# Kernel tuning notes

Hardware: AMD Instinct MI355X
Metric: run time of the kernel (lower is better)

Reference implementation:

```python
import jax, jax.numpy as jnp
import numpy as np

B, HID, REC, NC, T = 512, 196, 488, 35, 120
BN_EPS = 1e-3


def _bn(x, g, b):
    # eval-mode CustomBatchNorm1d: running_mean=0, running_var=1
    return g * (x / jnp.sqrt(1.0 + BN_EPS)) + b


def _gru(x, Wih, Whh, bih, bhh):
    """Standard torch nn.GRU (batch_first), h0 = 0. x: [B,T,D] -> [B,T,H]."""
    H = Whh.shape[1]
    def step(h, xt):
        xg = xt @ Wih.T + bih          # [B,3H]
        hg = h @ Whh.T + bhh           # [B,3H]
        xr, xz, xn = jnp.split(xg, 3, axis=1)
        hr, hz, hn = jnp.split(hg, 3, axis=1)
        r = jax.nn.sigmoid(xr + hr)
        z = jax.nn.sigmoid(xz + hz)
        n = jnp.tanh(xn + r * hn)
        h2 = (1.0 - z) * n + z * h
        return h2, h2
    h0 = jnp.zeros((x.shape[0], H), x.dtype)
    _, ys = jax.lax.scan(step, h0, jnp.swapaxes(x, 0, 1))
    return jnp.swapaxes(ys, 0, 1)


def _custom_gru(x, Wih, Whh, bih):
    """CustomGRUCell (eval mode: prev_target=0 so weight_tf term vanishes)."""
    H = Whh.shape[1]
    Whh_rz = Whh[:2 * H]
    Whh_n = Whh[2 * H:]
    b_r, b_z, b_n = bih[:H], bih[H:2 * H], bih[2 * H:]
    def step(h, xt):
        xg = xt @ Wih.T                 # [B,3H], no bias in F.linear
        xr, xz, xn = jnp.split(xg, 3, axis=1)
        hg = h @ Whh_rz.T               # only r,z rows needed (h_h chunk unused)
        hr, hz = jnp.split(hg, 2, axis=1)
        r = jax.nn.sigmoid(xr + hr + b_r)
        u = jax.nn.sigmoid(xz + hz + b_z)
        n = jax.nn.softmax(xn + (r * h) @ Whh_n.T + b_n, axis=1)
        h2 = (1.0 - u) * n + u * h
        return h2, h2
    h0 = jnp.zeros((x.shape[0], H), x.dtype)
    _, ys = jax.lax.scan(step, h0, jnp.swapaxes(x, 0, 1))
    return jnp.swapaxes(ys, 0, 1)


def setup_inputs() -> dict:
    key = jax.random.key(0)
    ks = jax.random.split(key, 16)
    s = 0.05
    inp = {
        "z_in": jax.random.normal(ks[0], (B, HID), jnp.float32),
        "W0": jax.random.normal(ks[1], (HID, HID), jnp.float32) * s,
        "b0": jnp.zeros((HID,), jnp.float32),
        "g0": jnp.full((1, HID), 0.1, jnp.float32),
        "beta0": jnp.zeros((1, HID), jnp.float32),
        "W1": jax.random.normal(ks[2], (HID, HID), jnp.float32) * s,
        "b1": jnp.zeros((HID,), jnp.float32),
        "g1": jnp.full((1, HID), 0.1, jnp.float32),
        "beta1": jnp.zeros((1, HID), jnp.float32),
        "gru0_Wih": jax.random.normal(ks[3], (3 * REC, HID), jnp.float32) * s,
        "gru0_Whh": jax.random.normal(ks[4], (3 * REC, REC), jnp.float32) * s,
        "gru0_bih": jax.random.normal(ks[5], (3 * REC,), jnp.float32) * s,
        "gru0_bhh": jax.random.normal(ks[6], (3 * REC,), jnp.float32) * s,
        "gru1_Wih": jax.random.normal(ks[7], (3 * REC, REC), jnp.float32) * s,
        "gru1_Whh": jax.random.normal(ks[8], (3 * REC, REC), jnp.float32) * s,
        "gru1_bih": jax.random.normal(ks[9], (3 * REC,), jnp.float32) * s,
        "gru1_bhh": jax.random.normal(ks[10], (3 * REC,), jnp.float32) * s,
        "cell_Wih": jax.random.normal(ks[11], (3 * NC, REC), jnp.float32) * s,
        "cell_Whh": jax.random.normal(ks[12], (3 * NC, NC), jnp.float32) * s,
        "cell_bih": jax.random.normal(ks[13], (3 * NC,), jnp.float32) * s,
    }
    return inp


def reference(z_in, W0, b0, g0, beta0, W1, b1, g1, beta1,
              gru0_Wih, gru0_Whh, gru0_bih, gru0_bhh,
              gru1_Wih, gru1_Whh, gru1_bih, gru1_bhh,
              cell_Wih, cell_Whh, cell_bih):
    z = _bn(z_in @ W0.T + b0, g0, beta0)
    z = _bn(z @ W1.T + b1, g1, beta1)
    z_reps = jnp.broadcast_to(z[:, None, :], (z.shape[0], T, z.shape[1]))
    x = _gru(z_reps, gru0_Wih, gru0_Whh, gru0_bih, gru0_bhh)
    x = _gru(x, gru1_Wih, gru1_Whh, gru1_bih, gru1_bhh)
    x_out = _custom_gru(x, cell_Wih, cell_Whh, cell_bih)  # [B,T,NCHARS]
    return x_out
```

## Files before the change

### kernel.cpp

```cpp
#include <hip/hip_runtime.h>
#include <math.h>

#define Bsz 512
#define HID 196
#define REC 488
#define NC  35
#define TT  120
#define G3  1464
#define NSLOT 123

#define KT   8
#define NCH  61
#define NB   61
#define CELLB 32
#define NGRID (3*NB + CELLB)
#define WSL  (NCH*KT*24)

#define HWREG_XCC_ID (20 | (0 << 6) | (31 << 11))

struct CellSmem { float xs[16][492]; float hs[16][36]; float rh[16][36]; };

__device__ __forceinline__ float sigmoidf_(float x) { return 1.0f / (1.0f + __expf(-x)); }

__device__ __forceinline__ void gbar(int* bar, int target) {
  __syncthreads();
  if (threadIdx.x == 0) {
    __builtin_amdgcn_fence(__ATOMIC_RELEASE, "agent");
    __hip_atomic_fetch_add(bar, 1, __ATOMIC_RELAXED, __HIP_MEMORY_SCOPE_AGENT);
    while (__hip_atomic_load(bar, __ATOMIC_RELAXED, __HIP_MEMORY_SCOPE_AGENT) < target)
      __builtin_amdgcn_s_sleep(2);
    __builtin_amdgcn_fence(__ATOMIC_ACQUIRE, "agent");
  }
  __syncthreads();
}

__device__ __forceinline__ void gbar2(int* bar, int xcd, int cntx, int nx, int s) {
  __syncthreads();
  if (threadIdx.x == 0) {
    int* bar1 = bar + 32*(1 + xcd);
    int old = __hip_atomic_fetch_add(bar1, 1, __ATOMIC_RELAXED, __HIP_MEMORY_SCOPE_AGENT);
    if (old == cntx*(s+1) - 1) {
      __builtin_amdgcn_fence(__ATOMIC_RELEASE, "agent");
      __hip_atomic_fetch_add(bar, 1, __ATOMIC_RELAXED, __HIP_MEMORY_SCOPE_AGENT);
    }
    while (__hip_atomic_load(bar, __ATOMIC_RELAXED, __HIP_MEMORY_SCOPE_AGENT) < nx*(s+1))
      __builtin_amdgcn_s_sleep(2);
    __builtin_amdgcn_fence(__ATOMIC_ACQUIRE, "agent");
  }
  __syncthreads();
}

__global__ void dense_bn_kernel(const float* __restrict__ X, const float* __restrict__ W,
                                const float* __restrict__ bias, const float* __restrict__ g,
                                const float* __restrict__ beta, float* __restrict__ Y) {
  __shared__ float xs[HID];
  int b = blockIdx.x;
  for (int k = threadIdx.x; k < HID; k += blockDim.x) xs[k] = X[(size_t)b*HID + k];
  __syncthreads();
  int j = threadIdx.x;
  if (j < HID) {
    const float4* wr = (const float4*)(W + (size_t)j*HID);
    float acc = 0.f;
    #pragma unroll 7
    for (int k4 = 0; k4 < HID/4; ++k4) {
      float4 w4 = wr[k4];
      acc += xs[4*k4+0]*w4.x + xs[4*k4+1]*w4.y + xs[4*k4+2]*w4.z + xs[4*k4+3]*w4.w;
    }
    float v = (acc + bias[j]) * 0.9995003746f;
    Y[(size_t)b*HID + j] = g[j]*v + beta[j];
  }
}

__global__ __launch_bounds__(256)
void xg0v2_kernel(const float* __restrict__ Z, const float* __restrict__ Wih,
                  const float* __restrict__ bih, float* __restrict__ XGT) {
  __shared__ float zs[HID*4];
  int b0 = blockIdx.x << 2;
  for (int idx = threadIdx.x; idx < HID*4; idx += 256) {
    int k = idx >> 2, i = idx & 3;
    zs[idx] = Z[(size_t)(b0+i)*HID + k];
  }
  __syncthreads();
  for (int c = threadIdx.x; c < G3; c += 256) {
    const float4* wr = (const float4*)(Wih + (size_t)c*HID);
    float a0=0.f,a1=0.f,a2=0.f,a3=0.f;
    for (int k4 = 0; k4 < HID/4; ++k4) {
      float4 w = wr[k4];
      const float* zp = zs + (k4<<4);
      a0=fmaf(w.x,zp[0],a0);  a1=fmaf(w.x,zp[1],a1);  a2=fmaf(w.x,zp[2],a2);  a3=fmaf(w.x,zp[3],a3);
      a0=fmaf(w.y,zp[4],a0);  a1=fmaf(w.y,zp[5],a1);  a2=fmaf(w.y,zp[6],a2);  a3=fmaf(w.y,zp[7],a3);
      a0=fmaf(w.z,zp[8],a0);  a1=fmaf(w.z,zp[9],a1);  a2=fmaf(w.z,zp[10],a2); a3=fmaf(w.z,zp[11],a3);
      a0=fmaf(w.w,zp[12],a0); a1=fmaf(w.w,zp[13],a1); a2=fmaf(w.w,zp[14],a2); a3=fmaf(w.w,zp[15],a3);
    }
    float bb = bih[c];
    XGT[(size_t)c*Bsz + b0+0] = a0 + bb;
    XGT[(size_t)c*Bsz + b0+1] = a1 + bb;
    XGT[(size_t)c*Bsz + b0+2] = a2 + bb;
    XGT[(size_t)c*Bsz + b0+3] = a3 + bb;
  }
}

__global__ __launch_bounds__(256)
void wtrans_kernel(const float* __restrict__ Whh0, const float* __restrict__ Wih1,
                   const float* __restrict__ Whh1, float* __restrict__ Wt2) {
  int blk = blockIdx.x;
  int stage = blk / NB, j = blk - stage*NB;
  const float* Wsrc = (stage==0) ? Whh0 : (stage==1) ? Wih1 : Whh1;
  float* dst = Wt2 + (size_t)blk*WSL;
  for (int idx = threadIdx.x; idx < WSL; idx += 256) {
    int ck = idx / 192, rem = idx - ck*192;
    int k = rem / 24, r = rem - k*24;
    int g = r >> 3, cl = r & 7;
    dst[idx] = Wsrc[(size_t)(g*REC + j*8 + cl)*REC + ck*8 + k];
  }
}

__device__ __forceinline__ void gemm24s(const float* __restrict__ AT, int b,
                                        const float* __restrict__ wp,
                                        float (&acc)[24])
{
  float av[KT], nv[KT];
  #pragma unroll
  for (int k = 0; k < KT; ++k) av[k] = AT[(size_t)k*Bsz + b];
  for (int ck = 0; ck < NCH; ++ck) {
    if (ck + 1 < NCH) {
      const float* src = AT + (size_t)(ck+1)*KT*Bsz + b;
      #pragma unroll
      for (int k = 0; k < KT; ++k) nv[k] = src[(size_t)k*Bsz];
    }
    const float* w = wp + ck*192;
    #pragma unroll
    for (int k = 0; k < KT; ++k) {
      float a = av[k];
      #pragma unroll
      for (int r = 0; r < 24; ++r)
        acc[r] = fmaf(a, w[k*24 + r], acc[r]);
    }
    #pragma unroll
    for (int k = 0; k < KT; ++k) av[k] = nv[k];
  }
}

__global__ __launch_bounds__(512)
void pers_kernel(const float* __restrict__ xg0T,
                 float* __restrict__ h0T, float* __restrict__ h1T,
                 float* __restrict__ xg1T, float* __restrict__ hc,
                 float* __restrict__ out,
                 const float* __restrict__ Wt2,
                 const float* __restrict__ bhh0,
                 const float* __restrict__ bih1, const float* __restrict__ bhh1,
                 const float* __restrict__ cWih, const float* __restrict__ cWhh,
                 const float* __restrict__ cb, int* __restrict__ bar)
{
  __shared__ CellSmem S;
  const int blk = blockIdx.x;
  const int tid = threadIdx.x;
  const int stage = (blk < NB) ? 0 : (blk < 2*NB) ? 1 : (blk < 3*NB) ? 2 : 3;
  const int l = tid & 63, w = tid >> 6;
  const float* wslice = Wt2 + (size_t)blk*WSL;

  const int xcd = __builtin_amdgcn_s_getreg(HWREG_XCC_ID) & 7;
  if (tid == 0)
    __hip_atomic_fetch_add(bar + 32*(9 + xcd), 1, __ATOMIC_RELAXED, __HIP_MEMORY_SCOPE_AGENT);
  gbar(bar + 544, NGRID);
  int cntx = 0, nx = 0;
  if (tid == 0) {
    cntx = __hip_atomic_load(bar + 32*(9 + xcd), __ATOMIC_RELAXED, __HIP_MEMORY_SCOPE_AGENT);
    #pragma unroll
    for (int x = 0; x < 8; ++x)
      nx += (__hip_atomic_load(bar + 32*(9 + x), __ATOMIC_RELAXED, __HIP_MEMORY_SCOPE_AGENT) > 0);
  }

  for (int s = 0; s < NSLOT; ++s) {
    if (stage == 0) {
      if (s < TT) {
        int j = blk;
        const float* hprevT = h0T + (size_t)((s+1)&1)*REC*Bsz;
        float*       hnewT  = h0T + (size_t)(s&1)*REC*Bsz;
        float acc[24] = {0};
        gemm24s(hprevT, tid, wslice, acc);
        int b = tid, c0 = j*8;
        #pragma unroll
        for (int cl = 0; cl < 8; ++cl) {
          int c = c0 + cl;
          float xrv = xg0T[(size_t)c*Bsz + b];
          float xzv = xg0T[(size_t)(REC+c)*Bsz + b];
          float xnv = xg0T[(size_t)(2*REC+c)*Bsz + b];
          float r = sigmoidf_(xrv + acc[cl]      + bhh0[c]);
          float z = sigmoidf_(xzv + acc[8+cl]    + bhh0[REC+c]);
          float n = tanhf   (xnv + r*(acc[16+cl] + bhh0[2*REC+c]));
          hnewT[(size_t)c*Bsz + b] = (1.f-z)*n + z*hprevT[(size_t)c*Bsz + b];
        }
      }
    } else if (stage == 1) {
      if (s >= 1 && s <= TT) {
        int t1 = s - 1;
        const float* xT   = h0T  + (size_t)(t1&1)*REC*Bsz;
        float*       xgwT = xg1T + (size_t)(t1&1)*G3*Bsz;
        float acc[24] = {0};
        gemm24s(xT, tid, wslice, acc);
        int b = tid, c0 = (blk - NB)*8;
        #pragma unroll
        for (int cl = 0; cl < 8; ++cl) {
          int c = c0 + cl;
          xgwT[(size_t)c*Bsz + b]         = acc[cl];
          xgwT[(size_t)(REC+c)*Bsz + b]   = acc[8+cl];
          xgwT[(size_t)(2*REC+c)*Bsz + b] = acc[16+cl];
        }
      }
    } else if (stage == 2) {
      if (s >= 2 && s <= TT+1) {
        int t2 = s - 2;
        const float* hprevT = h1T  + (size_t)((t2+1)&1)*REC*Bsz;
        float*       hnewT  = h1T  + (size_t)(t2&1)*REC*Bsz;
        const float* xgrT   = xg1T + (size_t)(t2&1)*G3*Bsz;
        float acc[24] = {0};
        gemm24s(hprevT, tid, wslice, acc);
        int b = tid, c0 = (blk - 2*NB)*8;
        #pragma unroll
        for (int cl = 0; cl < 8; ++cl) {
          int c = c0 + cl;
          float xrv = xgrT[(size_t)c*Bsz + b];
          float xzv = xgrT[(size_t)(REC+c)*Bsz + b];
          float xnv = xgrT[(size_t)(2*REC+c)*Bsz + b];
          float r = sigmoidf_(xrv + acc[cl]   + bih1[c]     + bhh1[c]);
          float z = sigmoidf_(xzv + acc[8+cl] + bih1[REC+c] + bhh1[REC+c]);
          float n = tanhf   (xnv + bih1[2*REC+c] + r*(acc[16+cl] + bhh1[2*REC+c]));
          hnewT[(size_t)c*Bsz + b] = (1.f-z)*n + z*hprevT[(size_t)c*Bsz + b];
        }
      }
    } else {
      if (s >= 3) {
        int t3 = s - 3;
        int b0 = (blk - 3*NB) << 4;
        const float* xT = h1T + (size_t)(t3&1)*REC*Bsz;
        const float* hp = hc  + (size_t)((t3+1)&1)*Bsz*NC;
        float*       hn = hc  + (size_t)(t3&1)*Bsz*NC;
        for (int idx = tid; idx < 16*REC; idx += 512) {
          int k = idx >> 4, it = idx & 15;
          S.xs[it][k] = xT[(size_t)k*Bsz + b0 + it];
        }
        if (l < NC) {
          #pragma unroll
          for (int q = 0; q < 2; ++q) {
            int it = (w<<1) + q;
            S.hs[it][l] = hp[(size_t)(b0+it)*NC + l];
          }
        }
        __syncthreads();
        for (int q = 0; q < 2; ++q) {
          int it = (w<<1) + q;
          int b = b0 + it;
          float v = -1e30f, u = 0.f, hpc = 0.f;
          if (l < NC) {
            const float4* wr4 = (const float4*)(cWih + (size_t)l*REC);
            const float4* wz4 = (const float4*)(cWih + (size_t)(NC+l)*REC);
            const float4* wn4 = (const float4*)(cWih + (size_t)(2*NC+l)*REC);
            const float4* xs4 = (const float4*)(S.xs[it]);
            float xr=0.f, xz=0.f, xn=0.f;
            #pragma unroll 2
            for (int k4 = 0; k4 < REC/4; ++k4) {
              float4 xv = xs4[k4];
              float4 wa = wr4[k4], wb = wz4[k4], wc = wn4[k4];
              xr += wa.x*xv.x + wa.y*xv.y + wa.z*xv.z + wa.w*xv.w;
              xz += wb.x*xv.x + wb.y*xv.y + wb.z*xv.z + wb.w*xv.w;
              xn += wc.x*xv.x + wc.y*xv.y + wc.z*xv.z + wc.w*xv.w;
            }
            float hr=0.f, hz=0.f;
            for (int k = 0; k < NC; ++k) {
              float hv = S.hs[it][k];
              hr = fmaf(hv, cWhh[(size_t)l*NC + k], hr);
              hz = fmaf(hv, cWhh[(size_t)(NC+l)*NC + k], hz);
            }
            float r = sigmoidf_(xr + hr + cb[l]);
            u       = sigmoidf_(xz + hz + cb[NC+l]);
            hpc = S.hs[it][l];
            S.rh[it][l] = r * hpc;
            v = xn;
          }
          __syncthreads();
          if (l < NC) {
            float hnn = 0.f;
            for (int k = 0; k < NC; ++k)
              hnn = fmaf(S.rh[it][k], cWhh[(size_t)(2*NC+l)*NC + k], hnn);
            v = v + hnn + cb[2*NC+l];
          }
          float m = v;
          #pragma unroll
          for (int o = 32; o; o >>= 1) m = fmaxf(m, __shfl_xor(m, o));
          float e = (l < NC) ? __expf(v - m) : 0.f;
          float ss = e;
          #pragma unroll
          for (int o = 32; o; o >>= 1) ss += __shfl_xor(ss, o);
          if (l < NC) {
            float h2 = (1.f - u)*(e/ss) + u*hpc;
            hn[(size_t)b*NC + l] = h2;
            out[((size_t)b*TT + t3)*NC + l] = h2;
          }
          __syncthreads();
        }
      }
    }
    gbar2(bar, xcd, cntx, nx, s);
  }
}

extern "C" void kernel_launch(void* const* d_in, const int* in_sizes, int n_in,
                              void* d_out, int out_size, void* d_ws, size_t ws_size,
                              hipStream_t stream) {
  const float* z_in  = (const float*)d_in[0];
  const float* W0    = (const float*)d_in[1];
  const float* b0    = (const float*)d_in[2];
  const float* g0    = (const float*)d_in[3];
  const float* beta0 = (const float*)d_in[4];
  const float* W1    = (const float*)d_in[5];
  const float* b1    = (const float*)d_in[6];
  const float* g1    = (const float*)d_in[7];
  const float* beta1 = (const float*)d_in[8];
  const float* Wih0  = (const float*)d_in[9];
  const float* Whh0  = (const float*)d_in[10];
  const float* bih0  = (const float*)d_in[11];
  const float* bhh0  = (const float*)d_in[12];
  const float* Wih1  = (const float*)d_in[13];
  const float* Whh1  = (const float*)d_in[14];
  const float* bih1  = (const float*)d_in[15];
  const float* bhh1  = (const float*)d_in[16];
  const float* cWih  = (const float*)d_in[17];
  const float* cWhh  = (const float*)d_in[18];
  const float* cbih  = (const float*)d_in[19];
  float* out = (float*)d_out;

  float* ws   = (float*)d_ws;
  int*   bar  = (int*)ws;
  float* h0T  = ws   + 1024;
  float* h1T  = h0T  + 2*(size_t)REC*Bsz;
  float* hcb  = h1T  + 2*(size_t)REC*Bsz;
  float* xg1T = hcb  + 2*(size_t)Bsz*NC;
  float* xg0T = xg1T + 2*(size_t)G3*Bsz;
  float* z1   = xg0T + (size_t)G3*Bsz;
  float* z2   = z1   + (size_t)Bsz*HID;
  float* Wt2  = z2   + (size_t)Bsz*HID;

  size_t zero_floats = 1024 + 4*(size_t)REC*Bsz + 2*(size_t)Bsz*NC;
  hipMemsetAsync(ws, 0, zero_floats*sizeof(float), stream);

  dense_bn_kernel<<<Bsz, 256, 0, stream>>>(z_in, W0, b0, g0, beta0, z1);
  dense_bn_kernel<<<Bsz, 256, 0, stream>>>(z1,   W1, b1, g1, beta1, z2);
  xg0v2_kernel   <<<128, 256, 0, stream>>>(z2, Wih0, bih0, xg0T);
  wtrans_kernel  <<<3*NB, 256, 0, stream>>>(Whh0, Wih1, Whh1, Wt2);

  pers_kernel<<<NGRID, 512, 0, stream>>>(xg0T, h0T, h1T, xg1T, hcb, out,
                                         Wt2, bhh0, bih1, bhh1, cWih, cWhh, cbih, bar);
}
```

Baseline: 11.09 ms.

## Split GRU recurrence K-loop across two thread halves with LDS reduction

The persistent kernel now launches 1024 threads per block. The two halves each compute part of the K chunks of the 24-column gate GEMM, and the second half's partial sums are reduced through shared memory before the gate math runs. The cell stage is packed into 16 blocks of 32 batch rows instead of 32 blocks of 16. This is meant to shorten the serial per-timestep GEMM latency on the recurrence critical path. In exchange it adds an extra block barrier, LDS traffic and tighter register limits at 1024 threads.

```diff
diff --git a/kernel.cpp b/kernel.cpp
--- a/kernel.cpp
+++ b/kernel.cpp
@@ -11,14 +11,16 @@
 
 #define KT   8
 #define NCH  61
+#define KSPL 31
 #define NB   61
-#define CELLB 32
+#define CELLB 16
 #define NGRID (3*NB + CELLB)
 #define WSL  (NCH*KT*24)
 
 #define HWREG_XCC_ID (20 | (0 << 6) | (31 << 11))
 
-struct CellSmem { float xs[16][492]; float hs[16][36]; float rh[16][36]; };
+struct CellSmem { float xs[32][492]; float hs[32][36]; float rh[32][36]; };
+union Smem { CellSmem cell; float red[512][28]; };
 
 __device__ __forceinline__ float sigmoidf_(float x) { return 1.0f / (1.0f + __expf(-x)); }
 
@@ -117,13 +119,14 @@
 
 __device__ __forceinline__ void gemm24s(const float* __restrict__ AT, int b,
                                         const float* __restrict__ wp,
-                                        float (&acc)[24])
+                                        float (&acc)[24], int c0, int c1)
 {
   float av[KT], nv[KT];
+  const float* s0 = AT + (size_t)c0*KT*Bsz + b;
   #pragma unroll
-  for (int k = 0; k < KT; ++k) av[k] = AT[(size_t)k*Bsz + b];
-  for (int ck = 0; ck < NCH; ++ck) {
-    if (ck + 1 < NCH) {
+  for (int k = 0; k < KT; ++k) av[k] = s0[(size_t)k*Bsz];
+  for (int ck = c0; ck < c1; ++ck) {
+    if (ck + 1 < c1) {
       const float* src = AT + (size_t)(ck+1)*KT*Bsz + b;
       #pragma unroll
       for (int k = 0; k < KT; ++k) nv[k] = src[(size_t)k*Bsz];
@@ -141,7 +144,7 @@
   }
 }
 
-__global__ __launch_bounds__(512)
+__global__ __launch_bounds__(1024)
 void pers_kernel(const float* __restrict__ xg0T,
                  float* __restrict__ h0T, float* __restrict__ h1T,
                  float* __restrict__ xg1T, float* __restrict__ hc,
@@ -152,10 +155,13 @@
                  const float* __restrict__ cWih, const float* __restrict__ cWhh,
                  const float* __restrict__ cb, int* __restrict__ bar)
 {
-  __shared__ CellSmem S;
+  __shared__ Smem S;
   const int blk = blockIdx.x;
   const int tid = threadIdx.x;
   const int stage = (blk < NB) ? 0 : (blk < 2*NB) ? 1 : (blk < 3*NB) ? 2 : 3;
+  const int b = tid & 511;
+  const int half = tid >> 9;
+  const int c0 = half ? KSPL : 0, c1 = half ? NCH : KSPL;
   const int l = tid & 63, w = tid >> 6;
   const float* wslice = Wt2 + (size_t)blk*WSL;
 
@@ -178,18 +184,33 @@
         const float* hprevT = h0T + (size_t)((s+1)&1)*REC*Bsz;
         float*       hnewT  = h0T + (size_t)(s&1)*REC*Bsz;
         float acc[24] = {0};
-        gemm24s(hprevT, tid, wslice, acc);
-        int b = tid, c0 = j*8;
-        #pragma unroll
-        for (int cl = 0; cl < 8; ++cl) {
-          int c = c0 + cl;
-          float xrv = xg0T[(size_t)c*Bsz + b];
-          float xzv = xg0T[(size_t)(REC+c)*Bsz + b];
-          float xnv = xg0T[(size_t)(2*REC+c)*Bsz + b];
-          float r = sigmoidf_(xrv + acc[cl]      + bhh0[c]);
-          float z = sigmoidf_(xzv + acc[8+cl]    + bhh0[REC+c]);
-          float n = tanhf   (xnv + r*(acc[16+cl] + bhh0[2*REC+c]));
-          hnewT[(size_t)c*Bsz + b] = (1.f-z)*n + z*hprevT[(size_t)c*Bsz + b];
+        gemm24s(hprevT, b, wslice, acc, c0, c1);
+        if (half) {
+          float4* dst = (float4*)S.red[b];
+          #pragma unroll
+          for (int q4 = 0; q4 < 6; ++q4)
+            dst[q4] = make_float4(acc[4*q4], acc[4*q4+1], acc[4*q4+2], acc[4*q4+3]);
+        }
+        __syncthreads();
+        if (!half) {
+          const float4* srcr = (const float4*)S.red[b];
+          #pragma unroll
+          for (int q4 = 0; q4 < 6; ++q4) {
+            float4 v = srcr[q4];
+            acc[4*q4] += v.x; acc[4*q4+1] += v.y; acc[4*q4+2] += v.z; acc[4*q4+3] += v.w;
+          }
+          int c0g = j*8;
+          #pragma unroll
+          for (int cl = 0; cl < 8; ++cl) {
+            int c = c0g + cl;
+            float xrv = xg0T[(size_t)c*Bsz + b];
+            float xzv = xg0T[(size_t)(REC+c)*Bsz + b];
+            float xnv = xg0T[(size_t)(2*REC+c)*Bsz + b];
+            float r = sigmoidf_(xrv + acc[cl]      + bhh0[c]);
+            float z = sigmoidf_(xzv + acc[8+cl]    + bhh0[REC+c]);
+            float n = tanhf   (xnv + r*(acc[16+cl] + bhh0[2*REC+c]));
+            hnewT[(size_t)c*Bsz + b] = (1.f-z)*n + z*hprevT[(size_t)c*Bsz + b];
+          }
         }
       }
     } else if (stage == 1) {
@@ -198,14 +219,29 @@
         const float* xT   = h0T  + (size_t)(t1&1)*REC*Bsz;
         float*       xgwT = xg1T + (size_t)(t1&1)*G3*Bsz;
         float acc[24] = {0};
-        gemm24s(xT, tid, wslice, acc);
-        int b = tid, c0 = (blk - NB)*8;
-        #pragma unroll
-        for (int cl = 0; cl < 8; ++cl) {
-          int c = c0 + cl;
-          xgwT[(size_t)c*Bsz + b]         = acc[cl];
-          xgwT[(size_t)(REC+c)*Bsz + b]   = acc[8+cl];
-          xgwT[(size_t)(2*REC+c)*Bsz + b] = acc[16+cl];
+        gemm24s(xT, b, wslice, acc, c0, c1);
+        if (half) {
+          float4* dst = (float4*)S.red[b];
+          #pragma unroll
+          for (int q4 = 0; q4 < 6; ++q4)
+            dst[q4] = make_float4(acc[4*q4], acc[4*q4+1], acc[4*q4+2], acc[4*q4+3]);
+        }
+        __syncthreads();
+        if (!half) {
+          const float4* srcr = (const float4*)S.red[b];
+          #pragma unroll
+          for (int q4 = 0; q4 < 6; ++q4) {
+            float4 v = srcr[q4];
+            acc[4*q4] += v.x; acc[4*q4+1] += v.y; acc[4*q4+2] += v.z; acc[4*q4+3] += v.w;
+          }
+          int c0g = (blk - NB)*8;
+          #pragma unroll
+          for (int cl = 0; cl < 8; ++cl) {
+            int c = c0g + cl;
+            xgwT[(size_t)c*Bsz + b]         = acc[cl];
+            xgwT[(size_t)(REC+c)*Bsz + b]   = acc[8+cl];
+            xgwT[(size_t)(2*REC+c)*Bsz + b] = acc[16+cl];
+          }
         }
       }
     } else if (stage == 2) {
@@ -215,48 +251,63 @@
         float*       hnewT  = h1T  + (size_t)(t2&1)*REC*Bsz;
         const float* xgrT   = xg1T + (size_t)(t2&1)*G3*Bsz;
         float acc[24] = {0};
-        gemm24s(hprevT, tid, wslice, acc);
-        int b = tid, c0 = (blk - 2*NB)*8;
-        #pragma unroll
-        for (int cl = 0; cl < 8; ++cl) {
-          int c = c0 + cl;
-          float xrv = xgrT[(size_t)c*Bsz + b];
-          float xzv = xgrT[(size_t)(REC+c)*Bsz + b];
-          float xnv = xgrT[(size_t)(2*REC+c)*Bsz + b];
-          float r = sigmoidf_(xrv + acc[cl]   + bih1[c]     + bhh1[c]);
-          float z = sigmoidf_(xzv + acc[8+cl] + bih1[REC+c] + bhh1[REC+c]);
-          float n = tanhf   (xnv + bih1[2*REC+c] + r*(acc[16+cl] + bhh1[2*REC+c]));
-          hnewT[(size_t)c*Bsz + b] = (1.f-z)*n + z*hprevT[(size_t)c*Bsz + b];
+        gemm24s(hprevT, b, wslice, acc, c0, c1);
+        if (half) {
+          float4* dst = (float4*)S.red[b];
+          #pragma unroll
+          for (int q4 = 0; q4 < 6; ++q4)
+            dst[q4] = make_float4(acc[4*q4], acc[4*q4+1], acc[4*q4+2], acc[4*q4+3]);
+        }
+        __syncthreads();
+        if (!half) {
+          const float4* srcr = (const float4*)S.red[b];
+          #pragma unroll
+          for (int q4 = 0; q4 < 6; ++q4) {
+            float4 v = srcr[q4];
+            acc[4*q4] += v.x; acc[4*q4+1] += v.y; acc[4*q4+2] += v.z; acc[4*q4+3] += v.w;
+          }
+          int c0g = (blk - 2*NB)*8;
+          #pragma unroll
+          for (int cl = 0; cl < 8; ++cl) {
+            int c = c0g + cl;
+            float xrv = xgrT[(size_t)c*Bsz + b];
+            float xzv = xgrT[(size_t)(REC+c)*Bsz + b];
+            float xnv = xgrT[(size_t)(2*REC+c)*Bsz + b];
+            float r = sigmoidf_(xrv + acc[cl]   + bih1[c]     + bhh1[c]);
+            float z = sigmoidf_(xzv + acc[8+cl] + bih1[REC+c] + bhh1[REC+c]);
+            float n = tanhf   (xnv + bih1[2*REC+c] + r*(acc[16+cl] + bhh1[2*REC+c]));
+            hnewT[(size_t)c*Bsz + b] = (1.f-z)*n + z*hprevT[(size_t)c*Bsz + b];
+          }
         }
       }
     } else {
       if (s >= 3) {
         int t3 = s - 3;
-        int b0 = (blk - 3*NB) << 4;
+        int b0 = (blk - 3*NB) << 5;
         const float* xT = h1T + (size_t)(t3&1)*REC*Bsz;
         const float* hp = hc  + (size_t)((t3+1)&1)*Bsz*NC;
         float*       hn = hc  + (size_t)(t3&1)*Bsz*NC;
-        for (int idx = tid; idx < 16*REC; idx += 512) {
-          int k = idx >> 4, it = idx & 15;
-          S.xs[it][k] = xT[(size_t)k*Bsz + b0 + it];
+        for (int idx = tid; idx < 32*REC; idx += 1024) {
+          int k = idx >> 5, it = idx & 31;
+          S.cell.xs[it][k] = xT[(size_t)k*Bsz + b0 + it];
         }
         if (l < NC) {
           #pragma unroll
           for (int q = 0; q < 2; ++q) {
             int it = (w<<1) + q;
-            S.hs[it][l] = hp[(size_t)(b0+it)*NC + l];
+            S.cell.hs[it][l] = hp[(size_t)(b0+it)*NC + l];
           }
         }
         __syncthreads();
         for (int q = 0; q < 2; ++q) {
           int it = (w<<1) + q;
-          int b = b0 + it;
+          int bb = b0 + it;
           float v = -1e30f, u = 0.f, hpc = 0.f;
           if (l < NC) {
             const float4* wr4 = (const float4*)(cWih + (size_t)l*REC);
             const float4* wz4 = (const float4*)(cWih + (size_t)(NC+l)*REC);
             const float4* wn4 = (const float4*)(cWih + (size_t)(2*NC+l)*REC);
-            const float4* xs4 = (const float4*)(S.xs[it]);
+            const float4* xs4 = (const float4*)(S.cell.xs[it]);
             float xr=0.f, xz=0.f, xn=0.f;
             #pragma unroll 2
             for (int k4 = 0; k4 < REC/4; ++k4) {
@@ -268,21 +319,21 @@
             }
             float hr=0.f, hz=0.f;
             for (int k = 0; k < NC; ++k) {
-              float hv = S.hs[it][k];
+              float hv = S.cell.hs[it][k];
               hr = fmaf(hv, cWhh[(size_t)l*NC + k], hr);
               hz = fmaf(hv, cWhh[(size_t)(NC+l)*NC + k], hz);
             }
             float r = sigmoidf_(xr + hr + cb[l]);
             u       = sigmoidf_(xz + hz + cb[NC+l]);
-            hpc = S.hs[it][l];
-            S.rh[it][l] = r * hpc;
+            hpc = S.cell.hs[it][l];
+            S.cell.rh[it][l] = r * hpc;
             v = xn;
           }
           __syncthreads();
           if (l < NC) {
             float hnn = 0.f;
             for (int k = 0; k < NC; ++k)
-              hnn = fmaf(S.rh[it][k], cWhh[(size_t)(2*NC+l)*NC + k], hnn);
+              hnn = fmaf(S.cell.rh[it][k], cWhh[(size_t)(2*NC+l)*NC + k], hnn);
             v = v + hnn + cb[2*NC+l];
           }
           float m = v;
@@ -294,8 +345,8 @@
           for (int o = 32; o; o >>= 1) ss += __shfl_xor(ss, o);
           if (l < NC) {
             float h2 = (1.f - u)*(e/ss) + u*hpc;
-            hn[(size_t)b*NC + l] = h2;
-            out[((size_t)b*TT + t3)*NC + l] = h2;
+            hn[(size_t)bb*NC + l] = h2;
+            out[((size_t)bb*TT + t3)*NC + l] = h2;
           }
           __syncthreads();
         }
@@ -349,6 +400,6 @@
   xg0v2_kernel   <<<128, 256, 0, stream>>>(z2, Wih0, bih0, xg0T);
   wtrans_kernel  <<<3*NB, 256, 0, stream>>>(Whh0, Wih1, Whh1, Wt2);
 
-  pers_kernel<<<NGRID, 512, 0, stream>>>(xg0T, h0T, h1T, xg1T, hcb, out,
-                                         Wt2, bhh0, bih1, bhh1, cWih, cWhh, cbih, bar);
-}
+  pers_kernel<<<NGRID, 1024, 0, stream>>>(xg0T, h0T, h1T, xg1T, hcb, out,
+                                          Wt2, bhh0, bih1, bhh1, cWih, cWhh, cbih, bar);
+}
```

Result: slower. 23.02 ms (+107.6%).
